# Kernel optimization log

Measured on AMD Instinct MI355X. Metric: run time of the kernel, lower is better.

## Reference

```python
import jax, jax.numpy as jnp
import numpy as np
import math

B, S, DM, H = 4, 4096, 1024, 16
HD = DM // H  # 64

def setup_inputs() -> dict:
    key = jax.random.key(0)
    ks = jax.random.split(key, 5)
    def xavier(k, shape):
        bound = math.sqrt(6.0 / (shape[0] + shape[1]))
        return jax.random.uniform(k, shape, jnp.float32, -bound, bound)
    return {
        "x": jax.random.normal(ks[0], (B, S, DM), jnp.float32),
        "Wq": xavier(ks[1], (DM, DM)),
        "Wk": xavier(ks[2], (DM, DM)),
        "Wv": xavier(ks[3], (DM, DM)),
        "Wfc": xavier(ks[4], (DM, DM)),
    }

def reference(x, Wq, Wk, Wv, Wfc):
    b, s, dm = x.shape
    h, hd = H, dm // H
    # nn.Linear(no bias): x @ W.T, then view [B, S, H, HD]
    Q = (x @ Wq.T).reshape(b, s, h, hd)
    K = (x @ Wk.T).reshape(b, s, h, hd)
    V = (x @ Wv.T).reshape(b, s, h, hd)
    # NOTE: faithful to original — no head transpose, so attention is over heads axis.
    # scores: [B, S, H, H]
    scores = jnp.einsum('bshd,bstd->bsht', Q, K) / math.sqrt(hd)
    attn = jax.nn.softmax(scores, axis=-1)
    # dropout is identity in eval mode
    out = jnp.einsum('bsht,bstd->bshd', attn, V).reshape(b, s, dm)
    return out @ Wfc.T
```

## Files before the change

### kernel.cpp

```cpp
#include <hip/hip_runtime.h>

typedef unsigned short u16;
typedef unsigned int u32;
typedef short bf16x8 __attribute__((ext_vector_type(8)));
typedef float f32x4 __attribute__((ext_vector_type(4)));

#define BM 128
#define BN 128

__device__ __forceinline__ u16 f2bf(float f) {
    u32 u = __float_as_uint(f);
    u32 r = (u + 0x7fffu + ((u >> 16) & 1u)) >> 16;
    return (u16)r;
}

__device__ __forceinline__ void unpack8(uint4 u, float* f) {
    f[0] = __uint_as_float(u.x << 16); f[1] = __uint_as_float(u.x & 0xffff0000u);
    f[2] = __uint_as_float(u.y << 16); f[3] = __uint_as_float(u.y & 0xffff0000u);
    f[4] = __uint_as_float(u.z << 16); f[5] = __uint_as_float(u.z & 0xffff0000u);
    f[6] = __uint_as_float(u.w << 16); f[7] = __uint_as_float(u.w & 0xffff0000u);
}

__device__ __forceinline__ void gld_lds16(const void* g, void* s) {
    __builtin_amdgcn_global_load_lds(
        (__attribute__((address_space(1))) void*)(g),
        (__attribute__((address_space(3))) void*)(s),
        16, 0, 0);
}

__global__ void cast_x_kernel(const float* __restrict__ s, u16* __restrict__ d, int n) {
    int i = (blockIdx.x * blockDim.x + threadIdx.x) * 4;
    if (i < n) {
        float4 v = *(const float4*)(s + i);
        ushort4 o;
        o.x = f2bf(v.x); o.y = f2bf(v.y); o.z = f2bf(v.z); o.w = f2bf(v.w);
        *(ushort4*)(d + i) = o;
    }
}

__global__ void cast_w_kernel(const float* __restrict__ wq, const float* __restrict__ wk,
                              const float* __restrict__ wv, const float* __restrict__ wfc,
                              u16* __restrict__ wqkv, u16* __restrict__ wfcb) {
    int y = blockIdx.y;
    const float* s = (y == 0) ? wq : (y == 1) ? wk : (y == 2) ? wv : wfc;
    u16* d = (y < 3) ? (wqkv + (size_t)y * (1u << 20)) : wfcb;
    int i = (blockIdx.x * blockDim.x + threadIdx.x) * 4;
    float4 v = *(const float4*)(s + i);
    ushort4 o;
    o.x = f2bf(v.x); o.y = f2bf(v.y); o.z = f2bf(v.z); o.w = f2bf(v.w);
    *(ushort4*)(d + i) = o;
}

template <int STOREF32>
__global__ __launch_bounds__(256, 2)
void gemm_bt(const u16* __restrict__ A, const u16* __restrict__ B,
             void* __restrict__ C, int M, int N, int K) {
    __shared__ __align__(16) u16 As[BM * 64];
    __shared__ __align__(16) u16 Bs[BN * 64];

    const int tid  = threadIdx.x;
    const int lane = tid & 63;
    const int wave = tid >> 6;
    const int wm = wave >> 1, wn = wave & 1;
    const int bm = blockIdx.y * BM;
    const int bn = blockIdx.x * BN;

    const int srow   = lane >> 3;
    const int schunk = (lane & 7) ^ srow;

    f32x4 acc[4][4];
#pragma unroll
    for (int i = 0; i < 4; ++i)
#pragma unroll
        for (int j = 0; j < 4; ++j) acc[i][j] = (f32x4){0.f, 0.f, 0.f, 0.f};

    const int nkt = K >> 6;
    for (int kt = 0; kt < nkt; ++kt) {
        const int k0 = kt << 6;
        __syncthreads();
#pragma unroll
        for (int j = 0; j < 4; ++j) {
            const int r = wave * 32 + j * 8;
            gld_lds16(A + (size_t)(bm + r + srow) * K + k0 + schunk * 8, &As[r * 64]);
            gld_lds16(B + (size_t)(bn + r + srow) * K + k0 + schunk * 8, &Bs[r * 64]);
        }
        __syncthreads();
#pragma unroll
        for (int kk = 0; kk < 2; ++kk) {
            const int c = kk * 4 + (lane >> 4);
            bf16x8 af[4], bfr[4];
#pragma unroll
            for (int i = 0; i < 4; ++i) {
                int m = wm * 64 + i * 16 + (lane & 15);
                af[i] = *(const bf16x8*)&As[m * 64 + ((c ^ (m & 7)) << 3)];
            }
#pragma unroll
            for (int j = 0; j < 4; ++j) {
                int n = wn * 64 + j * 16 + (lane & 15);
                bfr[j] = *(const bf16x8*)&Bs[n * 64 + ((c ^ (n & 7)) << 3)];
            }
#pragma unroll
            for (int i = 0; i < 4; ++i)
#pragma unroll
                for (int j = 0; j < 4; ++j)
                    acc[i][j] = __builtin_amdgcn_mfma_f32_16x16x32_bf16(
                        af[i], bfr[j], acc[i][j], 0, 0, 0);
        }
    }

    const int cr = (lane >> 4) * 4;
    const int cc = lane & 15;
#pragma unroll
    for (int i = 0; i < 4; ++i) {
#pragma unroll
        for (int j = 0; j < 4; ++j) {
            const int row0 = bm + wm * 64 + i * 16 + cr;
            const int col  = bn + wn * 64 + j * 16 + cc;
#pragma unroll
            for (int r = 0; r < 4; ++r) {
                float v = acc[i][j][r];
                size_t idx = (size_t)(row0 + r) * N + col;
                if (STOREF32) ((float*)C)[idx] = v;
                else          ((u16*)C)[idx]   = f2bf(v);
            }
        }
    }
}

__global__ __launch_bounds__(256)
void attn_kernel(const u16* __restrict__ QKV, u16* __restrict__ O) {
    __shared__ __align__(16) u16 sq[4][3][16 * 72];
    __shared__ float sp[4][16 * 20];

    const int lane = threadIdx.x & 63;
    const int wave = threadIdx.x >> 6;
    const size_t m = (size_t)blockIdx.x * 4 + wave;
    const u16* base = QKV + m * 3072;

#pragma unroll
    for (int c6 = 0; c6 < 6; ++c6) {
        int chunk = c6 * 64 + lane;
        int mat = chunk >> 7;
        int cc  = chunk & 127;
        int row = cc >> 3, pch = cc & 7;
        *(uint4*)&sq[wave][mat][row * 72 + pch * 8] = *(const uint4*)(base + chunk * 8);
    }
    __syncthreads();

    const int h = lane & 15, g = lane >> 4;
    float s[4] = {0.f, 0.f, 0.f, 0.f};
#pragma unroll
    for (int c = 0; c < 8; ++c) {
        uint4 qc = *(const uint4*)&sq[wave][0][h * 72 + c * 8];
        float qf[8]; unpack8(qc, qf);
#pragma unroll
        for (int t4 = 0; t4 < 4; ++t4) {
            int t = g * 4 + t4;
            uint4 kc = *(const uint4*)&sq[wave][1][t * 72 + c * 8];
            float kf[8]; unpack8(kc, kf);
#pragma unroll
            for (int e = 0; e < 8; ++e) s[t4] = fmaf(qf[e], kf[e], s[t4]);
        }
    }
#pragma unroll
    for (int t4 = 0; t4 < 4; ++t4) s[t4] *= 0.125f;

    float mx = fmaxf(fmaxf(s[0], s[1]), fmaxf(s[2], s[3]));
    mx = fmaxf(mx, __shfl_xor(mx, 16));
    mx = fmaxf(mx, __shfl_xor(mx, 32));
    float e[4], sum = 0.f;
#pragma unroll
    for (int t4 = 0; t4 < 4; ++t4) { e[t4] = __expf(s[t4] - mx); sum += e[t4]; }
    sum += __shfl_xor(sum, 16);
    sum += __shfl_xor(sum, 32);
    const float inv = 1.f / sum;
#pragma unroll
    for (int t4 = 0; t4 < 4; ++t4) sp[wave][h * 20 + g * 4 + t4] = e[t4] * inv;
    __syncthreads();

    const int h2 = h, dc = g;
    float o[16];
#pragma unroll
    for (int e2 = 0; e2 < 16; ++e2) o[e2] = 0.f;
#pragma unroll
    for (int t = 0; t < 16; ++t) {
        float pv = sp[wave][h2 * 20 + t];
        uint4 v0 = *(const uint4*)&sq[wave][2][t * 72 + dc * 16];
        uint4 v1 = *(const uint4*)&sq[wave][2][t * 72 + dc * 16 + 8];
        float vf[16]; unpack8(v0, vf); unpack8(v1, vf + 8);
#pragma unroll
        for (int e2 = 0; e2 < 16; ++e2) o[e2] = fmaf(pv, vf[e2], o[e2]);
    }
    u16 ob[16];
#pragma unroll
    for (int e2 = 0; e2 < 16; ++e2) ob[e2] = f2bf(o[e2]);
    uint4* dst = (uint4*)(O + m * 1024 + h2 * 64 + dc * 16);
    dst[0] = ((uint4*)ob)[0];
    dst[1] = ((uint4*)ob)[1];
}

extern "C" void kernel_launch(void* const* d_in, const int* in_sizes, int n_in,
                              void* d_out, int out_size, void* d_ws, size_t ws_size,
                              hipStream_t stream) {
    const float* x   = (const float*)d_in[0];
    const float* Wq  = (const float*)d_in[1];
    const float* Wk  = (const float*)d_in[2];
    const float* Wv  = (const float*)d_in[3];
    const float* Wfc = (const float*)d_in[4];
    float* out = (float*)d_out;

    const int M = 16384, K = 1024, NQKV = 3072, N2 = 1024;

    char* ws = (char*)d_ws;
    u16* xb    = (u16*)ws;
    u16* wqkvb = (u16*)(ws + 33554432);
    u16* wfcb  = (u16*)(ws + 33554432 + 6291456);
    u16* qkv   = (u16*)(ws + 33554432 + 6291456 + 2097152);

    cast_x_kernel<<<16384, 256, 0, stream>>>(x, xb, M * K);
    cast_w_kernel<<<dim3(1024, 4), 256, 0, stream>>>(Wq, Wk, Wv, Wfc, wqkvb, wfcb);

    gemm_bt<0><<<dim3(NQKV / BN, M / BM), 256, 0, stream>>>(xb, wqkvb, qkv, M, NQKV, K);

    u16* Ob = xb;
    attn_kernel<<<M / 4, 256, 0, stream>>>(qkv, Ob);

    gemm_bt<1><<<dim3(N2 / BN, M / BM), 256, 0, stream>>>(Ob, wfcb, out, M, N2, K);
}
```

Before: 323.1 us.

## Use MFMA for per-position head attention and merge cast kernels into one launch

The attention kernel now computes the 16x16 head-score matrix and the P·V product with bf16 MFMA instructions instead of scalar FMAs over unpacked bf16 values. V is stored transposed and swizzled in LDS, and probabilities are rounded to bf16. The separate x and weight cast kernels are merged into a single launch to save one kernel launch. Rounding the probabilities to bf16 adds a small precision loss, and the scattered 2-byte LDS writes for the V transpose add store traffic.

```diff
diff --git a/kernel.cpp b/kernel.cpp
--- a/kernel.cpp
+++ b/kernel.cpp
@@ -12,13 +12,6 @@
     u32 u = __float_as_uint(f);
     u32 r = (u + 0x7fffu + ((u >> 16) & 1u)) >> 16;
     return (u16)r;
-}
-
-__device__ __forceinline__ void unpack8(uint4 u, float* f) {
-    f[0] = __uint_as_float(u.x << 16); f[1] = __uint_as_float(u.x & 0xffff0000u);
-    f[2] = __uint_as_float(u.y << 16); f[3] = __uint_as_float(u.y & 0xffff0000u);
-    f[4] = __uint_as_float(u.z << 16); f[5] = __uint_as_float(u.z & 0xffff0000u);
-    f[6] = __uint_as_float(u.w << 16); f[7] = __uint_as_float(u.w & 0xffff0000u);
 }
 
 __device__ __forceinline__ void gld_lds16(const void* g, void* s) {
@@ -28,27 +21,27 @@
         16, 0, 0);
 }
 
-__global__ void cast_x_kernel(const float* __restrict__ s, u16* __restrict__ d, int n) {
-    int i = (blockIdx.x * blockDim.x + threadIdx.x) * 4;
-    if (i < n) {
-        float4 v = *(const float4*)(s + i);
-        ushort4 o;
-        o.x = f2bf(v.x); o.y = f2bf(v.y); o.z = f2bf(v.z); o.w = f2bf(v.w);
-        *(ushort4*)(d + i) = o;
-    }
-}
-
-__global__ void cast_w_kernel(const float* __restrict__ wq, const float* __restrict__ wk,
-                              const float* __restrict__ wv, const float* __restrict__ wfc,
-                              u16* __restrict__ wqkv, u16* __restrict__ wfcb) {
-    int y = blockIdx.y;
-    const float* s = (y == 0) ? wq : (y == 1) ? wk : (y == 2) ? wv : wfc;
-    u16* d = (y < 3) ? (wqkv + (size_t)y * (1u << 20)) : wfcb;
-    int i = (blockIdx.x * blockDim.x + threadIdx.x) * 4;
-    float4 v = *(const float4*)(s + i);
+__global__ void cast_all(const float* __restrict__ x,
+                         const float* __restrict__ wq, const float* __restrict__ wk,
+                         const float* __restrict__ wv, const float* __restrict__ wfc,
+                         u16* __restrict__ xb, u16* __restrict__ wqkvb, u16* __restrict__ wfcb) {
+    size_t g = (size_t)blockIdx.x * 256 + threadIdx.x;
+    const float* s;
+    u16* d;
+    size_t off;
+    if (g < 4194304u) {
+        s = x; d = xb; off = g;
+    } else {
+        size_t w = g - 4194304u;
+        int y = (int)(w >> 18);
+        off = w & 262143u;
+        s = (y == 0) ? wq : (y == 1) ? wk : (y == 2) ? wv : wfc;
+        d = (y < 3) ? (wqkvb + (size_t)y * 1048576u) : wfcb;
+    }
+    float4 v = ((const float4*)s)[off];
     ushort4 o;
     o.x = f2bf(v.x); o.y = f2bf(v.y); o.z = f2bf(v.z); o.w = f2bf(v.w);
-    *(ushort4*)(d + i) = o;
+    *(ushort4*)(d + off * 4) = o;
 }
 
 template <int STOREF32>
@@ -129,8 +122,10 @@
 
 __global__ __launch_bounds__(256)
 void attn_kernel(const u16* __restrict__ QKV, u16* __restrict__ O) {
-    __shared__ __align__(16) u16 sq[4][3][16 * 72];
-    __shared__ float sp[4][16 * 20];
+    __shared__ __align__(16) u16 sQ[4][16 * 80];
+    __shared__ __align__(16) u16 sK[4][16 * 80];
+    __shared__ __align__(16) u16 sV[4][64 * 16];
+    __shared__ __align__(16) u16 sP[4][16 * 16];
 
     const int lane = threadIdx.x & 63;
     const int wave = threadIdx.x >> 6;
@@ -138,65 +133,77 @@
     const u16* base = QKV + m * 3072;
 
 #pragma unroll
-    for (int c6 = 0; c6 < 6; ++c6) {
+    for (int c6 = 0; c6 < 4; ++c6) {
         int chunk = c6 * 64 + lane;
-        int mat = chunk >> 7;
-        int cc  = chunk & 127;
+        uint4 v = *(const uint4*)(base + chunk * 8);
+        int cc = chunk & 127;
         int row = cc >> 3, pch = cc & 7;
-        *(uint4*)&sq[wave][mat][row * 72 + pch * 8] = *(const uint4*)(base + chunk * 8);
+        u16* dst = (chunk < 128) ? sQ[wave] : sK[wave];
+        *(uint4*)&dst[row * 80 + pch * 8] = v;
+    }
+#pragma unroll
+    for (int c6 = 0; c6 < 2; ++c6) {
+        int cc = c6 * 64 + lane;
+        int t = cc >> 3, d0 = (cc & 7) * 8;
+        uint4 v = *(const uint4*)(base + 2048 + cc * 8);
+        u16 e[8]; *(uint4*)e = v;
+#pragma unroll
+        for (int k = 0; k < 8; ++k) {
+            int d = d0 + k;
+            int blk = (t >> 3) ^ ((d >> 3) & 1);
+            sV[wave][d * 16 + blk * 8 + (t & 7)] = e[k];
+        }
     }
     __syncthreads();
 
-    const int h = lane & 15, g = lane >> 4;
-    float s[4] = {0.f, 0.f, 0.f, 0.f};
-#pragma unroll
-    for (int c = 0; c < 8; ++c) {
-        uint4 qc = *(const uint4*)&sq[wave][0][h * 72 + c * 8];
-        float qf[8]; unpack8(qc, qf);
-#pragma unroll
-        for (int t4 = 0; t4 < 4; ++t4) {
-            int t = g * 4 + t4;
-            uint4 kc = *(const uint4*)&sq[wave][1][t * 72 + c * 8];
-            float kf[8]; unpack8(kc, kf);
-#pragma unroll
-            for (int e = 0; e < 8; ++e) s[t4] = fmaf(qf[e], kf[e], s[t4]);
-        }
-    }
-#pragma unroll
-    for (int t4 = 0; t4 < 4; ++t4) s[t4] *= 0.125f;
-
-    float mx = fmaxf(fmaxf(s[0], s[1]), fmaxf(s[2], s[3]));
+    const int ln = lane & 15;
+    const int g  = lane >> 4;
+
+    f32x4 s = (f32x4){0.f, 0.f, 0.f, 0.f};
+    {
+        bf16x8 a0 = *(const bf16x8*)&sK[wave][ln * 80 + g * 8];
+        bf16x8 b0 = *(const bf16x8*)&sQ[wave][ln * 80 + g * 8];
+        s = __builtin_amdgcn_mfma_f32_16x16x32_bf16(a0, b0, s, 0, 0, 0);
+        bf16x8 a1 = *(const bf16x8*)&sK[wave][ln * 80 + 32 + g * 8];
+        bf16x8 b1 = *(const bf16x8*)&sQ[wave][ln * 80 + 32 + g * 8];
+        s = __builtin_amdgcn_mfma_f32_16x16x32_bf16(a1, b1, s, 0, 0, 0);
+    }
+    float sv[4];
+#pragma unroll
+    for (int r = 0; r < 4; ++r) sv[r] = s[r] * 0.125f;
+
+    float mx = fmaxf(fmaxf(sv[0], sv[1]), fmaxf(sv[2], sv[3]));
     mx = fmaxf(mx, __shfl_xor(mx, 16));
     mx = fmaxf(mx, __shfl_xor(mx, 32));
     float e[4], sum = 0.f;
 #pragma unroll
-    for (int t4 = 0; t4 < 4; ++t4) { e[t4] = __expf(s[t4] - mx); sum += e[t4]; }
+    for (int r = 0; r < 4; ++r) { e[r] = __expf(sv[r] - mx); sum += e[r]; }
     sum += __shfl_xor(sum, 16);
     sum += __shfl_xor(sum, 32);
     const float inv = 1.f / sum;
-#pragma unroll
-    for (int t4 = 0; t4 < 4; ++t4) sp[wave][h * 20 + g * 4 + t4] = e[t4] * inv;
+
+    ushort4 pb;
+    pb.x = f2bf(e[0] * inv); pb.y = f2bf(e[1] * inv);
+    pb.z = f2bf(e[2] * inv); pb.w = f2bf(e[3] * inv);
+    *(ushort4*)&sP[wave][ln * 16 + g * 4] = pb;
     __syncthreads();
 
-    const int h2 = h, dc = g;
-    float o[16];
-#pragma unroll
-    for (int e2 = 0; e2 < 16; ++e2) o[e2] = 0.f;
-#pragma unroll
-    for (int t = 0; t < 16; ++t) {
-        float pv = sp[wave][h2 * 20 + t];
-        uint4 v0 = *(const uint4*)&sq[wave][2][t * 72 + dc * 16];
-        uint4 v1 = *(const uint4*)&sq[wave][2][t * 72 + dc * 16 + 8];
-        float vf[16]; unpack8(v0, vf); unpack8(v1, vf + 8);
-#pragma unroll
-        for (int e2 = 0; e2 < 16; ++e2) o[e2] = fmaf(pv, vf[e2], o[e2]);
-    }
-    u16 ob[16];
-#pragma unroll
-    for (int e2 = 0; e2 < 16; ++e2) ob[e2] = f2bf(o[e2]);
-    uint4* dst = (uint4*)(O + m * 1024 + h2 * 64 + dc * 16);
-    dst[0] = ((uint4*)ob)[0];
-    dst[1] = ((uint4*)ob)[1];
+    bf16x8 bl = *(const bf16x8*)&sP[wave][ln * 16 + (g & 1) * 8];
+    bf16x8 bz = (bf16x8){0, 0, 0, 0, 0, 0, 0, 0};
+    bf16x8 bp = (g < 2) ? bl : bz;
+
+#pragma unroll
+    for (int dt = 0; dt < 4; ++dt) {
+        int d = dt * 16 + ln;
+        int blk = (g & 1) ^ ((d >> 3) & 1);
+        bf16x8 av = *(const bf16x8*)&sV[wave][d * 16 + blk * 8];
+        f32x4 o = __builtin_amdgcn_mfma_f32_16x16x32_bf16(
+            av, bp, (f32x4){0.f, 0.f, 0.f, 0.f}, 0, 0, 0);
+        ushort4 ob;
+        ob.x = f2bf(o[0]); ob.y = f2bf(o[1]);
+        ob.z = f2bf(o[2]); ob.w = f2bf(o[3]);
+        *(ushort4*)(O + m * 1024 + ln * 64 + dt * 16 + g * 4) = ob;
+    }
 }
 
 extern "C" void kernel_launch(void* const* d_in, const int* in_sizes, int n_in,
@@ -217,8 +224,7 @@
     u16* wfcb  = (u16*)(ws + 33554432 + 6291456);
     u16* qkv   = (u16*)(ws + 33554432 + 6291456 + 2097152);
 
-    cast_x_kernel<<<16384, 256, 0, stream>>>(x, xb, M * K);
-    cast_w_kernel<<<dim3(1024, 4), 256, 0, stream>>>(Wq, Wk, Wv, Wfc, wqkvb, wfcb);
+    cast_all<<<20480, 256, 0, stream>>>(x, Wq, Wk, Wv, Wfc, xb, wqkvb, wfcb);
 
     gemm_bt<0><<<dim3(NQKV / BN, M / BM), 256, 0, stream>>>(xb, wqkvb, qkv, M, NQKV, K);
 
```

Measured after the change: 301.9 us. 1.07x faster.
